# Optimization experiments

Measured on AMD Instinct MI355X. Metric: run time of the kernel, lower is better.

Reference implementation:

```python
import jax, jax.numpy as jnp
import numpy as np

RBF_DIM = 64          # args.radius_emb_dim
FOLD_DIM = 128        # args.fold_dim
PROT_RADIUS = 30.0    # args.protein_radius (GaussianSmearing stop)
NP_, NL_, E_ = 100000, 50000, 500000


def gaussian_smearing(d):
    # GaussianSmearing(start=0, stop=PROT_RADIUS, num_gaussians=RBF_DIM)
    offsets = jnp.linspace(0.0, PROT_RADIUS, RBF_DIM, dtype=d.dtype)  # [R]
    coeff = -0.5 / (offsets[1] - offsets[0]) ** 2
    return jnp.exp(coeff * (d[:, None] - offsets[None, :]) ** 2)  # [E, R]


def setup_inputs() -> dict:
    key = jax.random.key(0)
    ks = jax.random.split(key, 12)
    scale = 10.0  # spread positions so distances span [0, PROT_RADIUS]
    pos = lambda k, n: jax.random.normal(k, (n, 3), jnp.float32) * scale
    inp = {
        'lig_pos': pos(ks[0], NL_),
        'prot_pos': pos(ks[1], NP_),
        'prot_pos_Cb': pos(ks[2], NP_),
        'prot_pos_C': pos(ks[3], NP_),
        'prot_pos_O': pos(ks[4], NP_),
        'prot_pos_N': pos(ks[5], NP_),
        'W1': jax.random.normal(ks[6], (5 * RBF_DIM, FOLD_DIM), jnp.float32) * 0.05,
        'b1': jnp.zeros((FOLD_DIM,), jnp.float32),
        'W2': jax.random.normal(ks[7], (FOLD_DIM, FOLD_DIM), jnp.float32) * 0.05,
        'b2': jnp.zeros((FOLD_DIM,), jnp.float32),
        'src': jax.random.randint(ks[8], (E_,), 0, NL_, jnp.int32),   # ligand index per edge
        'dst': jax.random.randint(ks[9], (E_,), 0, NP_, jnp.int32),   # protein index per edge
    }
    return inp


def reference(lig_pos, prot_pos, prot_pos_Cb, prot_pos_C, prot_pos_O, prot_pos_N,
              W1, b1, W2, b2, src, dst):
    lp = lig_pos[src]  # [E, 3] gather of ligand positions
    # 5 distance channels: CA/Cb/C/O/N protein atoms, each RBF-smeared
    feats = [gaussian_smearing(jnp.linalg.norm(lp - p[dst], axis=-1))
             for p in (prot_pos, prot_pos_Cb, prot_pos_C, prot_pos_O, prot_pos_N)]
    edge_attr = jnp.concatenate(feats, axis=-1)  # [E, 5*RBF_DIM]
    h = jax.nn.relu(edge_attr @ W1 + b1)         # [E, FOLD_DIM]
    return h @ W2 + b2                           # [E, FOLD_DIM]
```

## Files before the change

### kernel.cpp

```cpp
#include <hip/hip_runtime.h>
#include <hip/hip_bf16.h>

typedef unsigned short ushort_t;
typedef unsigned int uint_t;
typedef __attribute__((ext_vector_type(8))) short short8;
typedef __attribute__((ext_vector_type(4))) float f32x4;
typedef __attribute__((ext_vector_type(2))) uint_t uint2_t;

#define FOLD 128
#define S_CONST 1.78357580f
#define DS_CONST 0.84932180f

__device__ __forceinline__ uint_t pkbf(float a, float b) {
    __hip_bfloat162 h2 = __float22bfloat162_rn(float2{a, b});
    uint_t u;
    __builtin_memcpy(&u, &h2, sizeof(u));
    return u;
}

__device__ __forceinline__ void softbar() {
    asm volatile("s_waitcnt lgkmcnt(0)" ::: "memory");
    __builtin_amdgcn_s_barrier();
    asm volatile("" ::: "memory");
}

#define TEDGE 32

__global__ __launch_bounds__(512, 4) void fused(
    const float* __restrict__ lig,
    const float* __restrict__ p0, const float* __restrict__ p1,
    const float* __restrict__ p2, const float* __restrict__ p3,
    const float* __restrict__ p4,
    const float* __restrict__ W1, const float* __restrict__ W2,
    const float* __restrict__ b1, const float* __restrict__ b2,
    const int* __restrict__ src, const int* __restrict__ dst,
    float* __restrict__ out, int E)
{
    __shared__ float d_lds[2][5][TEDGE];
    __shared__ alignas(16) uint_t attrU[TEDGE * 160];
    __shared__ alignas(16) uint_t h_u[TEDGE * 64];
    __shared__ alignas(16) float out_s[TEDGE * FOLD];

    const int t = threadIdx.x;
    const int w = t >> 6;
    const int l = t & 63;
    const int lrow = l & 15, lgrp = l >> 4;
    const int aswz = (lrow & 7) << 2;
    const int ntiles = (E + TEDGE - 1) / TEDGE;
    const int G = gridDim.x;

    short8 wb1[10], wb2[4];
    #pragma unroll
    for (int ks = 0; ks < 10; ++ks) {
        uint_t dwv[4];
        #pragma unroll
        for (int jj = 0; jj < 4; ++jj) {
            float wa = W1[(ks * 32 + lgrp * 8 + 2 * jj)     * FOLD + w * 16 + lrow];
            float wc = W1[(ks * 32 + lgrp * 8 + 2 * jj + 1) * FOLD + w * 16 + lrow];
            dwv[jj] = pkbf(wa, wc);
        }
        __builtin_memcpy(&wb1[ks], dwv, 16);
    }
    #pragma unroll
    for (int ks = 0; ks < 4; ++ks) {
        uint_t dwv[4];
        #pragma unroll
        for (int jj = 0; jj < 4; ++jj) {
            float wa = W2[(ks * 32 + lgrp * 8 + 2 * jj)     * FOLD + w * 16 + lrow];
            float wc = W2[(ks * 32 + lgrp * 8 + 2 * jj + 1) * FOLD + w * 16 + lrow];
            dwv[jj] = pkbf(wa, wc);
        }
        __builtin_memcpy(&wb2[ks], dwv, 16);
    }
    f32x4 hb1 = *reinterpret_cast<const f32x4*>(&b1[w * 16 + lgrp * 4]);
    f32x4 hb2 = *reinterpret_cast<const f32x4*>(&b2[w * 16 + lgrp * 4]);

    const bool gth = (t < 160);
    const int g1c = t >> 5, g1m = t & 31;
    const float* GP = (g1c == 0) ? p0 : (g1c == 1) ? p1 : (g1c == 2) ? p2 : (g1c == 3) ? p3 : p4;

    const int m2 = t >> 4, q2 = t & 15;
    const int swz = (m2 & 7) << 2;
    const float ubase = (float)(4 * q2) * DS_CONST;

    int tile = blockIdx.x;
    if (tile >= ntiles) return;

    if (gth) {
        int e = tile * TEDGE + g1m; if (e >= E) e = E - 1;
        int s = src[e], dd = dst[e];
        float dx = lig[3 * s]     - GP[3 * dd];
        float dy = lig[3 * s + 1] - GP[3 * dd + 1];
        float dz = lig[3 * s + 2] - GP[3 * dd + 2];
        d_lds[0][g1c][g1m] = sqrtf(dx * dx + dy * dy + dz * dz);
    }
    int sN = 0, dN = 0;
    if (gth && tile + G < ntiles) {
        int e = (tile + G) * TEDGE + g1m; if (e >= E) e = E - 1;
        sN = src[e]; dN = dst[e];
    }
    softbar();

    int buf = 0;
    while (true) {
        const int next = tile + G;
        const bool havenext = (next < ntiles);

        float ax, ay, az, bx, by, bz;
        if (gth && havenext) {
            ax = lig[3 * sN];     bx = GP[3 * dN];
            ay = lig[3 * sN + 1]; by = GP[3 * dN + 1];
            az = lig[3 * sN + 2]; bz = GP[3 * dN + 2];
        }
        int sN2 = sN, dN2 = dN;
        if (gth && next + G < ntiles) {
            int e = (next + G) * TEDGE + g1m; if (e >= E) e = E - 1;
            sN2 = src[e]; dN2 = dst[e];
        }

        {
            float dv[5];
            #pragma unroll
            for (int c = 0; c < 5; ++c) dv[c] = d_lds[buf][c][m2];
            #pragma unroll
            for (int c = 0; c < 5; ++c) {
                float u0 = __builtin_fmaf(dv[c], S_CONST, -ubase);
                float u1 = u0 - DS_CONST;
                float u2 = u0 - 2.0f * DS_CONST;
                float u3 = u0 - 3.0f * DS_CONST;
                float v0 = __builtin_amdgcn_exp2f(-(u0 * u0));
                float v1 = __builtin_amdgcn_exp2f(-(u1 * u1));
                float v2 = __builtin_amdgcn_exp2f(-(u2 * u2));
                float v3 = __builtin_amdgcn_exp2f(-(u3 * u3));
                uint2_t pv;
                pv[0] = pkbf(v0, v1);
                pv[1] = pkbf(v2, v3);
                int o = 32 * c + 2 * q2;
                *reinterpret_cast<uint2_t*>(&attrU[m2 * 160 + (o ^ swz)]) = pv;
            }
        }
        softbar();

        f32x4 g1[2] = {{0.f,0.f,0.f,0.f},{0.f,0.f,0.f,0.f}};
        #pragma unroll
        for (int ks = 0; ks < 10; ++ks) {
            int o = ks * 16 + lgrp * 4;
            short8 af0 = *reinterpret_cast<const short8*>(&attrU[lrow * 160 + (o ^ aswz)]);
            short8 af1 = *reinterpret_cast<const short8*>(&attrU[(lrow + 16) * 160 + (o ^ aswz)]);
            g1[0] = __builtin_amdgcn_mfma_f32_16x16x32_bf16(wb1[ks], af0, g1[0], 0, 0, 0);
            g1[1] = __builtin_amdgcn_mfma_f32_16x16x32_bf16(wb1[ks], af1, g1[1], 0, 0, 0);
        }

        #pragma unroll
        for (int eh = 0; eh < 2; ++eh) {
            float v0 = fmaxf(g1[eh][0] + hb1[0], 0.f);
            float v1 = fmaxf(g1[eh][1] + hb1[1], 0.f);
            float v2 = fmaxf(g1[eh][2] + hb1[2], 0.f);
            float v3 = fmaxf(g1[eh][3] + hb1[3], 0.f);
            uint2_t pv;
            pv[0] = pkbf(v0, v1);
            pv[1] = pkbf(v2, v3);
            int e = eh * 16 + lrow;
            int dw = (w * 8 + lgrp * 2) ^ ((e & 7) << 2);
            *reinterpret_cast<uint2_t*>(&h_u[e * 64 + dw]) = pv;
        }

        if (gth && havenext) {
            float dx = ax - bx, dy = ay - by, dz = az - bz;
            d_lds[buf ^ 1][g1c][g1m] = sqrtf(dx * dx + dy * dy + dz * dz);
        }
        sN = sN2; dN = dN2;
        softbar();

        f32x4 o2[2] = {{0.f,0.f,0.f,0.f},{0.f,0.f,0.f,0.f}};
        #pragma unroll
        for (int ks = 0; ks < 4; ++ks) {
            int dw = ks * 16 + lgrp * 4;
            short8 hf0 = *reinterpret_cast<const short8*>(&h_u[lrow * 64 + (dw ^ aswz)]);
            short8 hf1 = *reinterpret_cast<const short8*>(&h_u[(lrow + 16) * 64 + (dw ^ aswz)]);
            o2[0] = __builtin_amdgcn_mfma_f32_16x16x32_bf16(wb2[ks], hf0, o2[0], 0, 0, 0);
            o2[1] = __builtin_amdgcn_mfma_f32_16x16x32_bf16(wb2[ks], hf1, o2[1], 0, 0, 0);
        }

        #pragma unroll
        for (int eh = 0; eh < 2; ++eh) {
            int e = eh * 16 + lrow;
            f32x4 v = o2[eh] + hb2;
            int ch4 = w * 4 + lgrp;
            *reinterpret_cast<f32x4*>(&out_s[e * FOLD + ((ch4 ^ (e & 7)) << 2)]) = v;
        }
        softbar();

        {
            int e_loc = t >> 4;
            if (tile * TEDGE + e_loc < E) {
                float* dp = out + (size_t)tile * TEDGE * FOLD + t * 8;
                #pragma unroll
                for (int k = 0; k < 2; ++k) {
                    int ch4 = (t & 15) * 2 + k;
                    f32x4 v = *reinterpret_cast<const f32x4*>(
                        &out_s[e_loc * FOLD + ((ch4 ^ (e_loc & 7)) << 2)]);
                    __builtin_nontemporal_store(v, reinterpret_cast<f32x4*>(dp) + k);
                }
            }
        }

        if (!havenext) break;
        tile = next;
        buf ^= 1;
    }
}

extern "C" void kernel_launch(void* const* d_in, const int* in_sizes, int n_in,
                              void* d_out, int out_size, void* d_ws, size_t ws_size,
                              hipStream_t stream) {
    const float* lig = (const float*)d_in[0];
    const float* p0  = (const float*)d_in[1];
    const float* p1  = (const float*)d_in[2];
    const float* p2  = (const float*)d_in[3];
    const float* p3  = (const float*)d_in[4];
    const float* p4  = (const float*)d_in[5];
    const float* W1  = (const float*)d_in[6];
    const float* b1  = (const float*)d_in[7];
    const float* W2  = (const float*)d_in[8];
    const float* b2  = (const float*)d_in[9];
    const int* src   = (const int*)d_in[10];
    const int* dst   = (const int*)d_in[11];
    float* out = (float*)d_out;
    const int E = in_sizes[10];

    int tiles = (E + TEDGE - 1) / TEDGE;
    int nblk = tiles < 512 ? tiles : 512;
    fused<<<nblk, 512, 0, stream>>>(lig, p0, p1, p2, p3, p4, W1, W2,
                                    b1, b2, src, dst, out, E);
}
```

Before: 123.2 us.

## Restructure to wave-per-tile processing with LDS-resident bf16 weights, no block barriers

Each wave now owns a whole 32-edge tile and computes all 128 output channels itself. Previously the 8 waves of a block split the output columns and synchronized through several block barriers per tile. Weights are packed to bf16 once into dynamic LDS (about 145 KB) and read as MFMA fragments. Gaussian features are built directly in registers using lane shuffles of distances, and outputs are stored straight to global without LDS staging. This removes per-tile block barriers and LDS round-trips for attributes and outputs, at the cost of large LDS use (one block per CU, 256 blocks), high register pressure from 16 accumulators, and repeated LDS weight reads per tile.

```diff
diff --git a/kernel.cpp b/kernel.cpp
--- a/kernel.cpp
+++ b/kernel.cpp
@@ -18,15 +18,15 @@
     return u;
 }
 
-__device__ __forceinline__ void softbar() {
-    asm volatile("s_waitcnt lgkmcnt(0)" ::: "memory");
-    __builtin_amdgcn_s_barrier();
-    asm volatile("" ::: "memory");
-}
-
-#define TEDGE 32
-
-__global__ __launch_bounds__(512, 4) void fused(
+#define NWAVES 8
+#define W1_OFF 0
+#define W2_OFF 20480
+#define B1_OFF 28672
+#define B2_OFF 28800
+#define H_OFF  28928
+#define LDS_DW 37120
+
+__global__ __launch_bounds__(512) void fused(
     const float* __restrict__ lig,
     const float* __restrict__ p0, const float* __restrict__ p1,
     const float* __restrict__ p2, const float* __restrict__ p3,
@@ -36,178 +36,178 @@
     const int* __restrict__ src, const int* __restrict__ dst,
     float* __restrict__ out, int E)
 {
-    __shared__ float d_lds[2][5][TEDGE];
-    __shared__ alignas(16) uint_t attrU[TEDGE * 160];
-    __shared__ alignas(16) uint_t h_u[TEDGE * 64];
-    __shared__ alignas(16) float out_s[TEDGE * FOLD];
+    extern __shared__ uint_t smem[];
+    uint_t* W1L = smem + W1_OFF;
+    uint_t* W2L = smem + W2_OFF;
+    const float* b1L = (const float*)(smem + B1_OFF);
+    const float* b2L = (const float*)(smem + B2_OFF);
 
     const int t = threadIdx.x;
     const int w = t >> 6;
     const int l = t & 63;
-    const int lrow = l & 15, lgrp = l >> 4;
-    const int aswz = (lrow & 7) << 2;
-    const int ntiles = (E + TEDGE - 1) / TEDGE;
-    const int G = gridDim.x;
-
-    short8 wb1[10], wb2[4];
-    #pragma unroll
-    for (int ks = 0; ks < 10; ++ks) {
-        uint_t dwv[4];
-        #pragma unroll
-        for (int jj = 0; jj < 4; ++jj) {
-            float wa = W1[(ks * 32 + lgrp * 8 + 2 * jj)     * FOLD + w * 16 + lrow];
-            float wc = W1[(ks * 32 + lgrp * 8 + 2 * jj + 1) * FOLD + w * 16 + lrow];
-            dwv[jj] = pkbf(wa, wc);
-        }
-        __builtin_memcpy(&wb1[ks], dwv, 16);
-    }
-    #pragma unroll
-    for (int ks = 0; ks < 4; ++ks) {
-        uint_t dwv[4];
-        #pragma unroll
-        for (int jj = 0; jj < 4; ++jj) {
-            float wa = W2[(ks * 32 + lgrp * 8 + 2 * jj)     * FOLD + w * 16 + lrow];
-            float wc = W2[(ks * 32 + lgrp * 8 + 2 * jj + 1) * FOLD + w * 16 + lrow];
-            dwv[jj] = pkbf(wa, wc);
-        }
-        __builtin_memcpy(&wb2[ks], dwv, 16);
-    }
-    f32x4 hb1 = *reinterpret_cast<const f32x4*>(&b1[w * 16 + lgrp * 4]);
-    f32x4 hb2 = *reinterpret_cast<const f32x4*>(&b2[w * 16 + lgrp * 4]);
-
-    const bool gth = (t < 160);
-    const int g1c = t >> 5, g1m = t & 31;
-    const float* GP = (g1c == 0) ? p0 : (g1c == 1) ? p1 : (g1c == 2) ? p2 : (g1c == 3) ? p3 : p4;
-
-    const int m2 = t >> 4, q2 = t & 15;
-    const int swz = (m2 & 7) << 2;
-    const float ubase = (float)(4 * q2) * DS_CONST;
-
-    int tile = blockIdx.x;
-    if (tile >= ntiles) return;
-
-    if (gth) {
-        int e = tile * TEDGE + g1m; if (e >= E) e = E - 1;
-        int s = src[e], dd = dst[e];
-        float dx = lig[3 * s]     - GP[3 * dd];
-        float dy = lig[3 * s + 1] - GP[3 * dd + 1];
-        float dz = lig[3 * s + 2] - GP[3 * dd + 2];
-        d_lds[0][g1c][g1m] = sqrtf(dx * dx + dy * dy + dz * dz);
-    }
-    int sN = 0, dN = 0;
-    if (gth && tile + G < ntiles) {
-        int e = (tile + G) * TEDGE + g1m; if (e >= E) e = E - 1;
-        sN = src[e]; dN = dst[e];
-    }
-    softbar();
-
-    int buf = 0;
+    const int eL = l & 15, g = l >> 4;
+    uint_t* hw = smem + H_OFF + (w << 10);
+
+    for (int idx = t; idx < 20480; idx += 512) {
+        int jj = idx & 3, l2 = (idx >> 2) & 63, nt = (idx >> 8) & 7, ks = idx >> 11;
+        int row = ks * 32 + ((l2 >> 4) << 3) + 2 * jj;
+        int col = nt * 16 + (l2 & 15);
+        W1L[idx] = pkbf(W1[row * FOLD + col], W1[(row + 1) * FOLD + col]);
+    }
+    for (int idx = t; idx < 8192; idx += 512) {
+        int jj = idx & 3, l2 = (idx >> 2) & 63, nt = (idx >> 8) & 7, ks = idx >> 11;
+        int row = ks * 32 + ((l2 >> 4) << 3) + 2 * jj;
+        int col = nt * 16 + (l2 & 15);
+        W2L[idx] = pkbf(W2[row * FOLD + col], W2[(row + 1) * FOLD + col]);
+    }
+    if (t < 128) ((float*)(smem + B1_OFF))[t] = b1[t];
+    else if (t < 256) ((float*)(smem + B2_OFF))[t - 128] = b2[t - 128];
+    __syncthreads();
+
+    const int NT = (E + 31) >> 5;
+    const int stride = gridDim.x * NWAVES;
+    int wt = blockIdx.x * NWAVES + w;
+    if (wt >= NT) return;
+
+    const float* GP = (g == 0) ? p0 : (g == 1) ? p1 : (g == 2) ? p2 : p3;
+    const bool g0 = (g == 0);
+    const float gbase = (float)(8 * g) * DS_CONST;
+
+    float Ax[2], Ay[2], Az[2], Px[2], Py[2], Pz[2], Qx[2], Qy[2], Qz[2];
+    {
+        #pragma unroll
+        for (int eh = 0; eh < 2; ++eh) {
+            int e = wt * 32 + eh * 16 + eL; if (e >= E) e = E - 1;
+            int s = src[e], d2 = dst[e];
+            Ax[eh] = lig[3 * s]; Ay[eh] = lig[3 * s + 1]; Az[eh] = lig[3 * s + 2];
+            Px[eh] = GP[3 * d2]; Py[eh] = GP[3 * d2 + 1]; Pz[eh] = GP[3 * d2 + 2];
+            if (g0) { Qx[eh] = p4[3 * d2]; Qy[eh] = p4[3 * d2 + 1]; Qz[eh] = p4[3 * d2 + 2]; }
+        }
+    }
+
     while (true) {
-        const int next = tile + G;
-        const bool havenext = (next < ntiles);
-
-        float ax, ay, az, bx, by, bz;
-        if (gth && havenext) {
-            ax = lig[3 * sN];     bx = GP[3 * dN];
-            ay = lig[3 * sN + 1]; by = GP[3 * dN + 1];
-            az = lig[3 * sN + 2]; bz = GP[3 * dN + 2];
-        }
-        int sN2 = sN, dN2 = dN;
-        if (gth && next + G < ntiles) {
-            int e = (next + G) * TEDGE + g1m; if (e >= E) e = E - 1;
-            sN2 = src[e]; dN2 = dst[e];
-        }
-
-        {
-            float dv[5];
-            #pragma unroll
-            for (int c = 0; c < 5; ++c) dv[c] = d_lds[buf][c][m2];
-            #pragma unroll
-            for (int c = 0; c < 5; ++c) {
-                float u0 = __builtin_fmaf(dv[c], S_CONST, -ubase);
-                float u1 = u0 - DS_CONST;
-                float u2 = u0 - 2.0f * DS_CONST;
-                float u3 = u0 - 3.0f * DS_CONST;
-                float v0 = __builtin_amdgcn_exp2f(-(u0 * u0));
-                float v1 = __builtin_amdgcn_exp2f(-(u1 * u1));
-                float v2 = __builtin_amdgcn_exp2f(-(u2 * u2));
-                float v3 = __builtin_amdgcn_exp2f(-(u3 * u3));
+        const int wt2 = wt + stride;
+        const bool more = (wt2 < NT);
+
+        int sB[2], dB[2];
+        if (more) {
+            #pragma unroll
+            for (int eh = 0; eh < 2; ++eh) {
+                int e = wt2 * 32 + eh * 16 + eL; if (e >= E) e = E - 1;
+                sB[eh] = src[e]; dB[eh] = dst[e];
+            }
+        }
+
+        float u00[5][2];
+        #pragma unroll
+        for (int eh = 0; eh < 2; ++eh) {
+            float dx = Ax[eh] - Px[eh], dy = Ay[eh] - Py[eh], dz = Az[eh] - Pz[eh];
+            float dm = sqrtf(dx * dx + dy * dy + dz * dz);
+            float d4 = 0.f;
+            if (g0) {
+                float ex = Ax[eh] - Qx[eh], ey = Ay[eh] - Qy[eh], ez = Az[eh] - Qz[eh];
+                d4 = sqrtf(ex * ex + ey * ey + ez * ez);
+            }
+            #pragma unroll
+            for (int c = 0; c < 4; ++c)
+                u00[c][eh] = __builtin_fmaf(__shfl(dm, c * 16 + eL), S_CONST, -gbase);
+            u00[4][eh] = __builtin_fmaf(__shfl(d4, eL), S_CONST, -gbase);
+        }
+
+        short8 a[2][10];
+        #pragma unroll
+        for (int ks = 0; ks < 10; ++ks) {
+            const int c = ks >> 1;
+            #pragma unroll
+            for (int eh = 0; eh < 2; ++eh) {
+                uint_t dwv[4];
+                #pragma unroll
+                for (int jj = 0; jj < 4; ++jj) {
+                    float k0 = (float)((ks & 1) * 32 + 2 * jj) * DS_CONST;
+                    float k1 = (float)((ks & 1) * 32 + 2 * jj + 1) * DS_CONST;
+                    float ua = u00[c][eh] - k0;
+                    float ub = u00[c][eh] - k1;
+                    float va = __builtin_amdgcn_exp2f(-(ua * ua));
+                    float vb = __builtin_amdgcn_exp2f(-(ub * ub));
+                    dwv[jj] = pkbf(va, vb);
+                }
+                __builtin_memcpy(&a[eh][ks], dwv, 16);
+            }
+        }
+
+        float Bx[2], By[2], Bz[2], Rx[2], Ry[2], Rz[2], Sx[2], Sy[2], Sz[2];
+        if (more) {
+            #pragma unroll
+            for (int eh = 0; eh < 2; ++eh) {
+                Bx[eh] = lig[3 * sB[eh]]; By[eh] = lig[3 * sB[eh] + 1]; Bz[eh] = lig[3 * sB[eh] + 2];
+                Rx[eh] = GP[3 * dB[eh]]; Ry[eh] = GP[3 * dB[eh] + 1]; Rz[eh] = GP[3 * dB[eh] + 2];
+                if (g0) { Sx[eh] = p4[3 * dB[eh]]; Sy[eh] = p4[3 * dB[eh] + 1]; Sz[eh] = p4[3 * dB[eh] + 2]; }
+            }
+        }
+
+        f32x4 acc1[8][2];
+        #pragma unroll
+        for (int nt = 0; nt < 8; ++nt)
+            #pragma unroll
+            for (int eh = 0; eh < 2; ++eh) acc1[nt][eh] = f32x4{0.f, 0.f, 0.f, 0.f};
+        #pragma unroll
+        for (int ks = 0; ks < 10; ++ks) {
+            #pragma unroll
+            for (int nt = 0; nt < 8; ++nt) {
+                const short8 wf = *reinterpret_cast<const short8*>(&W1L[((ks * 8 + nt) * 64 + l) * 4]);
+                acc1[nt][0] = __builtin_amdgcn_mfma_f32_16x16x32_bf16(wf, a[0][ks], acc1[nt][0], 0, 0, 0);
+                acc1[nt][1] = __builtin_amdgcn_mfma_f32_16x16x32_bf16(wf, a[1][ks], acc1[nt][1], 0, 0, 0);
+            }
+        }
+
+        const int swzE = (eL & 7) << 3;
+        #pragma unroll
+        for (int eh = 0; eh < 2; ++eh) {
+            #pragma unroll
+            for (int nt = 0; nt < 8; ++nt) {
+                f32x4 bv = *reinterpret_cast<const f32x4*>(&b1L[nt * 16 + g * 4]);
+                float v0 = fmaxf(acc1[nt][eh][0] + bv[0], 0.f);
+                float v1 = fmaxf(acc1[nt][eh][1] + bv[1], 0.f);
+                float v2 = fmaxf(acc1[nt][eh][2] + bv[2], 0.f);
+                float v3 = fmaxf(acc1[nt][eh][3] + bv[3], 0.f);
                 uint2_t pv;
                 pv[0] = pkbf(v0, v1);
                 pv[1] = pkbf(v2, v3);
-                int o = 32 * c + 2 * q2;
-                *reinterpret_cast<uint2_t*>(&attrU[m2 * 160 + (o ^ swz)]) = pv;
-            }
-        }
-        softbar();
-
-        f32x4 g1[2] = {{0.f,0.f,0.f,0.f},{0.f,0.f,0.f,0.f}};
-        #pragma unroll
-        for (int ks = 0; ks < 10; ++ks) {
-            int o = ks * 16 + lgrp * 4;
-            short8 af0 = *reinterpret_cast<const short8*>(&attrU[lrow * 160 + (o ^ aswz)]);
-            short8 af1 = *reinterpret_cast<const short8*>(&attrU[(lrow + 16) * 160 + (o ^ aswz)]);
-            g1[0] = __builtin_amdgcn_mfma_f32_16x16x32_bf16(wb1[ks], af0, g1[0], 0, 0, 0);
-            g1[1] = __builtin_amdgcn_mfma_f32_16x16x32_bf16(wb1[ks], af1, g1[1], 0, 0, 0);
-        }
-
-        #pragma unroll
-        for (int eh = 0; eh < 2; ++eh) {
-            float v0 = fmaxf(g1[eh][0] + hb1[0], 0.f);
-            float v1 = fmaxf(g1[eh][1] + hb1[1], 0.f);
-            float v2 = fmaxf(g1[eh][2] + hb1[2], 0.f);
-            float v3 = fmaxf(g1[eh][3] + hb1[3], 0.f);
-            uint2_t pv;
-            pv[0] = pkbf(v0, v1);
-            pv[1] = pkbf(v2, v3);
-            int e = eh * 16 + lrow;
-            int dw = (w * 8 + lgrp * 2) ^ ((e & 7) << 2);
-            *reinterpret_cast<uint2_t*>(&h_u[e * 64 + dw]) = pv;
-        }
-
-        if (gth && havenext) {
-            float dx = ax - bx, dy = ay - by, dz = az - bz;
-            d_lds[buf ^ 1][g1c][g1m] = sqrtf(dx * dx + dy * dy + dz * dz);
-        }
-        sN = sN2; dN = dN2;
-        softbar();
-
-        f32x4 o2[2] = {{0.f,0.f,0.f,0.f},{0.f,0.f,0.f,0.f}};
-        #pragma unroll
-        for (int ks = 0; ks < 4; ++ks) {
-            int dw = ks * 16 + lgrp * 4;
-            short8 hf0 = *reinterpret_cast<const short8*>(&h_u[lrow * 64 + (dw ^ aswz)]);
-            short8 hf1 = *reinterpret_cast<const short8*>(&h_u[(lrow + 16) * 64 + (dw ^ aswz)]);
-            o2[0] = __builtin_amdgcn_mfma_f32_16x16x32_bf16(wb2[ks], hf0, o2[0], 0, 0, 0);
-            o2[1] = __builtin_amdgcn_mfma_f32_16x16x32_bf16(wb2[ks], hf1, o2[1], 0, 0, 0);
-        }
-
-        #pragma unroll
-        for (int eh = 0; eh < 2; ++eh) {
-            int e = eh * 16 + lrow;
-            f32x4 v = o2[eh] + hb2;
-            int ch4 = w * 4 + lgrp;
-            *reinterpret_cast<f32x4*>(&out_s[e * FOLD + ((ch4 ^ (e & 7)) << 2)]) = v;
-        }
-        softbar();
-
-        {
-            int e_loc = t >> 4;
-            if (tile * TEDGE + e_loc < E) {
-                float* dp = out + (size_t)tile * TEDGE * FOLD + t * 8;
+                *reinterpret_cast<uint2_t*>(&hw[eL * 64 + ((nt * 8 + g * 2) ^ swzE)]) = pv;
+            }
+            f32x4 acc2[8];
+            #pragma unroll
+            for (int nt = 0; nt < 8; ++nt) acc2[nt] = f32x4{0.f, 0.f, 0.f, 0.f};
+            #pragma unroll
+            for (int ks2 = 0; ks2 < 4; ++ks2) {
+                const short8 hf = *reinterpret_cast<const short8*>(&hw[eL * 64 + ((ks2 * 16 + g * 4) ^ swzE)]);
                 #pragma unroll
-                for (int k = 0; k < 2; ++k) {
-                    int ch4 = (t & 15) * 2 + k;
-                    f32x4 v = *reinterpret_cast<const f32x4*>(
-                        &out_s[e_loc * FOLD + ((ch4 ^ (e_loc & 7)) << 2)]);
-                    __builtin_nontemporal_store(v, reinterpret_cast<f32x4*>(dp) + k);
+                for (int nt = 0; nt < 8; ++nt) {
+                    const short8 wf2 = *reinterpret_cast<const short8*>(&W2L[((ks2 * 8 + nt) * 64 + l) * 4]);
+                    acc2[nt] = __builtin_amdgcn_mfma_f32_16x16x32_bf16(wf2, hf, acc2[nt], 0, 0, 0);
                 }
             }
-        }
-
-        if (!havenext) break;
-        tile = next;
-        buf ^= 1;
+            int e = wt * 32 + eh * 16 + eL;
+            if (e < E) {
+                #pragma unroll
+                for (int nt = 0; nt < 8; ++nt) {
+                    f32x4 bv2 = *reinterpret_cast<const f32x4*>(&b2L[nt * 16 + g * 4]);
+                    f32x4 v = acc2[nt] + bv2;
+                    __builtin_nontemporal_store(v,
+                        reinterpret_cast<f32x4*>(&out[(size_t)e * FOLD + nt * 16 + g * 4]));
+                }
+            }
+            asm volatile("s_waitcnt lgkmcnt(0)" ::: "memory");
+        }
+
+        if (!more) break;
+        wt = wt2;
+        #pragma unroll
+        for (int eh = 0; eh < 2; ++eh) {
+            Ax[eh] = Bx[eh]; Ay[eh] = By[eh]; Az[eh] = Bz[eh];
+            Px[eh] = Rx[eh]; Py[eh] = Ry[eh]; Pz[eh] = Rz[eh];
+            if (g0) { Qx[eh] = Sx[eh]; Qy[eh] = Sy[eh]; Qz[eh] = Sz[eh]; }
+        }
     }
 }
 
@@ -229,8 +229,10 @@
     float* out = (float*)d_out;
     const int E = in_sizes[10];
 
-    int tiles = (E + TEDGE - 1) / TEDGE;
-    int nblk = tiles < 512 ? tiles : 512;
-    fused<<<nblk, 512, 0, stream>>>(lig, p0, p1, p2, p3, p4, W1, W2,
-                                    b1, b2, src, dst, out, E);
+    hipFuncSetAttribute(reinterpret_cast<const void*>(fused),
+                        hipFuncAttributeMaxDynamicSharedMemorySize, LDS_DW * 4);
+
+    int nblk = 256;
+    fused<<<nblk, 512, LDS_DW * 4, stream>>>(lig, p0, p1, p2, p3, p4, W1, W2,
+                                             b1, b2, src, dst, out, E);
 }
```

Result: faster. 109.3 us (-11.3%).
